# Optimization experiments

Measured on AMD Instinct MI355X. Metric: run time of the kernel, lower is better.

## Reference

```python
import jax, jax.numpy as jnp
import numpy as np
from jax import lax


def setup_inputs() -> dict:
    key = jax.random.key(0)
    k1, k2, k3, k4, k5 = jax.random.split(key, 5)
    B, T, D, N = 64, 1024, 512, 24
    return {
        "x": jax.random.normal(k1, (B, T, D), dtype=jnp.float32),
        "W": jax.random.normal(k2, (D, N), dtype=jnp.float32) * 0.05,
        "b": jnp.zeros((N,), dtype=jnp.float32),
        "trans": jax.random.normal(k3, (N, N), dtype=jnp.float32) * 0.1,
        "left_boundary": jax.random.normal(k4, (N,), dtype=jnp.float32) * 0.1,
        "right_boundary": jax.random.normal(k5, (N,), dtype=jnp.float32) * 0.1,
    }


def reference(x, W, b, trans, left_boundary, right_boundary):
    # Dense projection to tag potentials: [B, T, N]
    pot = jnp.einsum("btd,dn->btn", x, W) + b
    B, T, N = pot.shape
    # mask=None -> lengths are all T; boundaries added at t=0 and t=T-1
    lens = jnp.full((B,), T, dtype=jnp.int32)
    pot = pot.at[:, 0, :].add(left_boundary).at[:, T - 1, :].add(right_boundary)

    # Viterbi forward: alpha[b, j] = best score of any path ending in tag j
    def fwd_step(alpha, pot_t):
        scores = alpha[:, :, None] + trans[None, :, :]  # [B, prev, cur]
        bp = jnp.argmax(scores, axis=1)                 # [B, N] best prev tag
        alpha_new = jnp.max(scores, axis=1) + pot_t
        return alpha_new, bp

    alpha0 = pot[:, 0, :]
    pot_rest = jnp.swapaxes(pot[:, 1:, :], 0, 1)  # [T-1, B, N]
    alpha_T, bps = lax.scan(fwd_step, alpha0, pot_rest)
    last_tag = jnp.argmax(alpha_T, axis=-1)  # [B]

    # Backtrack through backpointers (reverse scan over time)
    def back_step(tag, bp_t):
        prev = jnp.take_along_axis(bp_t, tag[:, None], axis=1)[:, 0]
        return prev, prev

    _, tags_head = lax.scan(back_step, last_tag, bps, reverse=True)  # [T-1, B]
    decoded = jnp.concatenate(
        [jnp.swapaxes(tags_head, 0, 1), last_tag[:, None]], axis=1
    ).astype(jnp.int32)  # [B, T]
    return decoded, pot, lens, trans
```

## Files before the change

### kernel.cpp

```cpp
#include <hip/hip_runtime.h>
#include <hip/hip_bf16.h>

#define BB 64
#define TT 1024
#define DD 512
#define NS 24

#define POT_OFF   65536
#define LENS_OFF  1638400
#define TRANS_OFF 1638464

__global__ __launch_bounds__(256, 4) void gemm_pot(
    const float* __restrict__ x, const float* __restrict__ W,
    const float* __restrict__ bias, const float* __restrict__ trans,
    const float* __restrict__ lb, const float* __restrict__ rb,
    float* __restrict__ out)
{
  __shared__ float red[3][64][25];
  const int tid = threadIdx.x;
  const int l   = tid & 63;
  const int q   = __builtin_amdgcn_readfirstlane(tid >> 6);
  const int row = blockIdx.x * 64 + l;

  const float4* xp = (const float4*)(x + (size_t)row * DD + q * 128);

  float acc[NS];
#pragma unroll
  for (int nn = 0; nn < NS; ++nn) acc[nn] = 0.f;

  float4 buf[16];
#pragma unroll
  for (int i = 0; i < 16; ++i) buf[i] = xp[i];

#pragma unroll
  for (int c = 0; c < 8; ++c) {
#pragma unroll
    for (int i = 0; i < 4; ++i) {
      const int f = c * 4 + i;
      const int s = f & 15;
      float4 v = buf[s];
      if (f + 16 < 32) buf[s] = xp[f + 16];
      const float* Wr = W + (size_t)(q * 128 + f * 4) * NS;
      const float x0 = v.x, x1 = v.y, x2 = v.z, x3 = v.w;
#pragma unroll
      for (int nn = 0; nn < NS; ++nn) acc[nn] = fmaf(x0, Wr[nn],          acc[nn]);
#pragma unroll
      for (int nn = 0; nn < NS; ++nn) acc[nn] = fmaf(x1, Wr[NS + nn],     acc[nn]);
#pragma unroll
      for (int nn = 0; nn < NS; ++nn) acc[nn] = fmaf(x2, Wr[2 * NS + nn], acc[nn]);
#pragma unroll
      for (int nn = 0; nn < NS; ++nn) acc[nn] = fmaf(x3, Wr[3 * NS + nn], acc[nn]);
    }
  }

  if (q != 0) {
#pragma unroll
    for (int nn = 0; nn < NS; ++nn) red[q - 1][l][nn] = acc[nn];
  }
  __syncthreads();
  if (q == 0) {
    const int t = row & (TT - 1);
#pragma unroll
    for (int nn = 0; nn < NS; ++nn)
      acc[nn] += red[0][l][nn] + red[1][l][nn] + red[2][l][nn] + bias[nn];
    if (t == 0) {
#pragma unroll
      for (int nn = 0; nn < NS; ++nn) acc[nn] += lb[nn];
    }
    if (t == TT - 1) {
#pragma unroll
      for (int nn = 0; nn < NS; ++nn) acc[nn] += rb[nn];
    }
    float* po = out + POT_OFF + (size_t)row * NS;
#pragma unroll
    for (int i = 0; i < 6; ++i)
      *(float4*)(po + i * 4) = make_float4(acc[4*i], acc[4*i+1], acc[4*i+2], acc[4*i+3]);
  }

  if (blockIdx.x == 0 && tid < BB) out[LENS_OFF + tid] = (float)TT;
  if (blockIdx.x == 1) {
    for (int i = tid; i < NS * NS; i += 256) out[TRANS_OFF + i] = trans[i];
  }
}

__global__ __launch_bounds__(1024) void viterbi_fused(
    const float* __restrict__ pot, const float* __restrict__ trans,
    float* __restrict__ out_dec)
{
  __shared__ float ps[(TT + 8) * NS];
  __shared__ unsigned char bl[TT * NS];
  __shared__ float tl[NS * NS];
  __shared__ int H[32][NS];
  __shared__ int e[32];

  const int b = blockIdx.x, tid = threadIdx.x;

  {
    const float4* src = (const float4*)(pot + (size_t)b * TT * NS);
    float4* dst = (float4*)ps;
#pragma unroll
    for (int i = 0; i < 6; ++i) dst[tid + i * 1024] = src[tid + i * 1024];
    if (tid < NS * NS) tl[tid] = trans[tid];
  }
  __syncthreads();

  if (tid < 24) {
    const int n = tid;
    float tc[NS];
#pragma unroll
    for (int m = 0; m < NS; ++m) tc[m] = tl[m * NS + n];

    float as_[NS];
    {
      const float4* ar = (const float4*)ps;
#pragma unroll
      for (int i = 0; i < 6; ++i) {
        float4 v = ar[i];
        as_[4*i] = v.x; as_[4*i+1] = v.y; as_[4*i+2] = v.z; as_[4*i+3] = v.w;
      }
    }

    float pv[8];
#pragma unroll
    for (int u = 0; u < 8; ++u) pv[u] = ps[(1 + u) * NS + n];

    auto step = [&](int tt, float potv) {
      float sc[NS];
#pragma unroll
      for (int m = 0; m < NS; ++m) sc[m] = as_[m] + tc[m];
      float r0 = fmaxf(fmaxf(sc[0],  sc[1]),  sc[2]);
      float r1 = fmaxf(fmaxf(sc[3],  sc[4]),  sc[5]);
      float r2 = fmaxf(fmaxf(sc[6],  sc[7]),  sc[8]);
      float r3 = fmaxf(fmaxf(sc[9],  sc[10]), sc[11]);
      float r4 = fmaxf(fmaxf(sc[12], sc[13]), sc[14]);
      float r5 = fmaxf(fmaxf(sc[15], sc[16]), sc[17]);
      float r6 = fmaxf(fmaxf(sc[18], sc[19]), sc[20]);
      float r7 = fmaxf(fmaxf(sc[21], sc[22]), sc[23]);
      float q0 = fmaxf(fmaxf(r0, r1), r2);
      float q1 = fmaxf(fmaxf(r3, r4), r5);
      float q2 = fmaxf(r6, r7);
      float best = fmaxf(fmaxf(q0, q1), q2);
      float anew = best + potv;
      ps[tt * NS + n] = anew;
      const float4* ar = (const float4*)(ps + tt * NS);
#pragma unroll
      for (int i = 0; i < 6; ++i) {
        float4 v = ar[i];
        as_[4*i] = v.x; as_[4*i+1] = v.y; as_[4*i+2] = v.z; as_[4*i+3] = v.w;
      }
    };

    for (int t = 1; t + 7 <= TT - 1; t += 8) {
#pragma unroll
      for (int u = 0; u < 8; ++u) {
        const int tt = t + u;
        const float potv = pv[u];
        pv[u] = ps[(tt + 8) * NS + n];
        step(tt, potv);
      }
    }
#pragma unroll
    for (int u = 0; u < 7; ++u) step(1017 + u, pv[u]);
  }
  __syncthreads();

  for (int idx = tid; idx < (TT - 1) * NS; idx += 1024) {
    const int n = idx % NS;
    const int t = idx / NS + 1;
    const float* ar = &ps[(t - 1) * NS];
    float best = ar[0] + tl[n];
    int bi = 0;
#pragma unroll
    for (int m = 1; m < NS; ++m) {
      float s = ar[m] + tl[m * NS + n];
      bool g = s > best;
      bi = g ? m : bi;
      best = g ? s : best;
    }
    bl[t * NS + n] = (unsigned char)bi;
  }
  __syncthreads();

  if (tid < 32 * NS) {
    const int c = tid / NS, s = tid % NS;
    int a = s;
    int tlo = c * 32; if (tlo < 1) tlo = 1;
    for (int t = c * 32 + 31; t >= tlo; --t) a = bl[t * NS + a];
    H[c][s] = a;
  }
  __syncthreads();

  if (tid == 0) {
    const float* ar = &ps[(TT - 1) * NS];
    float best = ar[0]; int bi = 0;
#pragma unroll
    for (int nn = 1; nn < NS; ++nn) {
      float v = ar[nn];
      if (v > best) { best = v; bi = nn; }
    }
    int tag = bi;
    e[31] = tag;
    for (int c = 31; c >= 1; --c) { tag = H[c][tag]; e[c - 1] = tag; }
  }
  __syncthreads();

  if (tid < 32) {
    const int c = tid;
    int tag = e[c];
    float* od = out_dec + (size_t)b * TT;
    od[c * 32 + 31] = (float)tag;
    for (int t = c * 32 + 30; t >= c * 32; --t) {
      tag = bl[(t + 1) * NS + tag];
      od[t] = (float)tag;
    }
  }
}

extern "C" void kernel_launch(void* const* d_in, const int* in_sizes, int n_in,
                              void* d_out, int out_size, void* d_ws, size_t ws_size,
                              hipStream_t stream)
{
  const float* x     = (const float*)d_in[0];
  const float* W     = (const float*)d_in[1];
  const float* bias  = (const float*)d_in[2];
  const float* trans = (const float*)d_in[3];
  const float* lb    = (const float*)d_in[4];
  const float* rb    = (const float*)d_in[5];
  float* out = (float*)d_out;

  gemm_pot<<<1024, 256, 0, stream>>>(x, W, bias, trans, lb, rb, out);
  viterbi_fused<<<BB, 1024, 0, stream>>>(out + POT_OFF, trans, out);
}
```

Measured before the change: 382.6 us.

## Stage W in LDS for GEMM and split Viterbi max across two half-waves

The projection kernel now copies the whole 512x24 weight matrix into shared memory once per block and reads it as float4 rows, instead of reading W from global memory for every FMA group. The x prefetch buffer shrinks to 8 entries, and the shared buffer is reused for the cross-wave reduction. The Viterbi forward recursion now uses 64 lanes: each half-wave computes the max over 12 predecessor tags and combines with its partner through ds_bpermute, shortening the serial per-step dependency chain. Costs are 48KB of LDS per GEMM block, which limits occupancy, and an extra permute on each serial step.

Result: faster. 330.5 us (-13.6%).

```diff
diff --git a/kernel.cpp b/kernel.cpp
--- a/kernel.cpp
+++ b/kernel.cpp
@@ -10,59 +10,67 @@
 #define LENS_OFF  1638400
 #define TRANS_OFF 1638464
 
-__global__ __launch_bounds__(256, 4) void gemm_pot(
+__global__ __launch_bounds__(256) void gemm_pot(
     const float* __restrict__ x, const float* __restrict__ W,
     const float* __restrict__ bias, const float* __restrict__ trans,
     const float* __restrict__ lb, const float* __restrict__ rb,
     float* __restrict__ out)
 {
-  __shared__ float red[3][64][25];
+  __shared__ float wl[DD * NS];
   const int tid = threadIdx.x;
   const int l   = tid & 63;
-  const int q   = __builtin_amdgcn_readfirstlane(tid >> 6);
+  const int q   = tid >> 6;
   const int row = blockIdx.x * 64 + l;
 
+  {
+    const float4* Ws = (const float4*)W;
+    float4* Wd = (float4*)wl;
+#pragma unroll
+    for (int i = 0; i < 12; ++i) Wd[tid + i * 256] = Ws[tid + i * 256];
+  }
+  __syncthreads();
+
   const float4* xp = (const float4*)(x + (size_t)row * DD + q * 128);
 
   float acc[NS];
 #pragma unroll
   for (int nn = 0; nn < NS; ++nn) acc[nn] = 0.f;
 
-  float4 buf[16];
-#pragma unroll
-  for (int i = 0; i < 16; ++i) buf[i] = xp[i];
-
-#pragma unroll
-  for (int c = 0; c < 8; ++c) {
-#pragma unroll
-    for (int i = 0; i < 4; ++i) {
-      const int f = c * 4 + i;
-      const int s = f & 15;
-      float4 v = buf[s];
-      if (f + 16 < 32) buf[s] = xp[f + 16];
-      const float* Wr = W + (size_t)(q * 128 + f * 4) * NS;
-      const float x0 = v.x, x1 = v.y, x2 = v.z, x3 = v.w;
-#pragma unroll
-      for (int nn = 0; nn < NS; ++nn) acc[nn] = fmaf(x0, Wr[nn],          acc[nn]);
-#pragma unroll
-      for (int nn = 0; nn < NS; ++nn) acc[nn] = fmaf(x1, Wr[NS + nn],     acc[nn]);
-#pragma unroll
-      for (int nn = 0; nn < NS; ++nn) acc[nn] = fmaf(x2, Wr[2 * NS + nn], acc[nn]);
-#pragma unroll
-      for (int nn = 0; nn < NS; ++nn) acc[nn] = fmaf(x3, Wr[3 * NS + nn], acc[nn]);
-    }
-  }
-
+  float4 buf[8];
+#pragma unroll
+  for (int i = 0; i < 8; ++i) buf[i] = xp[i];
+
+#pragma unroll
+  for (int f = 0; f < 32; ++f) {
+    float4 v = buf[f & 7];
+    if (f + 8 < 32) buf[f & 7] = xp[f + 8];
+    const float xj[4] = {v.x, v.y, v.z, v.w};
+#pragma unroll
+    for (int j = 0; j < 4; ++j) {
+      const int k = q * 128 + f * 4 + j;
+      const float4* wr = (const float4*)&wl[k * NS];
+      float4 w0 = wr[0], w1 = wr[1], w2 = wr[2], w3 = wr[3], w4 = wr[4], w5 = wr[5];
+      const float wv[NS] = {w0.x,w0.y,w0.z,w0.w, w1.x,w1.y,w1.z,w1.w,
+                            w2.x,w2.y,w2.z,w2.w, w3.x,w3.y,w3.z,w3.w,
+                            w4.x,w4.y,w4.z,w4.w, w5.x,w5.y,w5.z,w5.w};
+      const float xv = xj[j];
+#pragma unroll
+      for (int nn = 0; nn < NS; ++nn) acc[nn] = fmaf(xv, wv[nn], acc[nn]);
+    }
+  }
+
+  __syncthreads();
   if (q != 0) {
 #pragma unroll
-    for (int nn = 0; nn < NS; ++nn) red[q - 1][l][nn] = acc[nn];
+    for (int nn = 0; nn < NS; ++nn) wl[((q - 1) * 64 + l) * 25 + nn] = acc[nn];
   }
   __syncthreads();
   if (q == 0) {
     const int t = row & (TT - 1);
 #pragma unroll
     for (int nn = 0; nn < NS; ++nn)
-      acc[nn] += red[0][l][nn] + red[1][l][nn] + red[2][l][nn] + bias[nn];
+      acc[nn] += wl[(0 * 64 + l) * 25 + nn] + wl[(1 * 64 + l) * 25 + nn]
+               + wl[(2 * 64 + l) * 25 + nn] + bias[nn];
     if (t == 0) {
 #pragma unroll
       for (int nn = 0; nn < NS; ++nn) acc[nn] += lb[nn];
@@ -104,19 +112,22 @@
   }
   __syncthreads();
 
-  if (tid < 24) {
-    const int n = tid;
-    float tc[NS];
-#pragma unroll
-    for (int m = 0; m < NS; ++m) tc[m] = tl[m * NS + n];
-
-    float as_[NS];
+  if (tid < 64) {
+    const int g  = tid >> 5;
+    const int n0 = tid & 31;
+    const int n  = (n0 < 24) ? n0 : 23;
+
+    float tc[12];
+#pragma unroll
+    for (int j = 0; j < 12; ++j) tc[j] = tl[(12 * g + j) * NS + n];
+
+    float as12[12];
     {
-      const float4* ar = (const float4*)ps;
-#pragma unroll
-      for (int i = 0; i < 6; ++i) {
-        float4 v = ar[i];
-        as_[4*i] = v.x; as_[4*i+1] = v.y; as_[4*i+2] = v.z; as_[4*i+3] = v.w;
+      const float4* rr = (const float4*)&ps[12 * g];
+#pragma unroll
+      for (int i = 0; i < 3; ++i) {
+        float4 v = rr[i];
+        as12[4*i] = v.x; as12[4*i+1] = v.y; as12[4*i+2] = v.z; as12[4*i+3] = v.w;
       }
     }
 
@@ -124,29 +135,26 @@
 #pragma unroll
     for (int u = 0; u < 8; ++u) pv[u] = ps[(1 + u) * NS + n];
 
+    const int partner = (tid ^ 32) * 4;
+
     auto step = [&](int tt, float potv) {
-      float sc[NS];
-#pragma unroll
-      for (int m = 0; m < NS; ++m) sc[m] = as_[m] + tc[m];
-      float r0 = fmaxf(fmaxf(sc[0],  sc[1]),  sc[2]);
-      float r1 = fmaxf(fmaxf(sc[3],  sc[4]),  sc[5]);
-      float r2 = fmaxf(fmaxf(sc[6],  sc[7]),  sc[8]);
-      float r3 = fmaxf(fmaxf(sc[9],  sc[10]), sc[11]);
-      float r4 = fmaxf(fmaxf(sc[12], sc[13]), sc[14]);
-      float r5 = fmaxf(fmaxf(sc[15], sc[16]), sc[17]);
-      float r6 = fmaxf(fmaxf(sc[18], sc[19]), sc[20]);
-      float r7 = fmaxf(fmaxf(sc[21], sc[22]), sc[23]);
-      float q0 = fmaxf(fmaxf(r0, r1), r2);
-      float q1 = fmaxf(fmaxf(r3, r4), r5);
-      float q2 = fmaxf(r6, r7);
-      float best = fmaxf(fmaxf(q0, q1), q2);
-      float anew = best + potv;
+      float sc[12];
+#pragma unroll
+      for (int j = 0; j < 12; ++j) sc[j] = as12[j] + tc[j];
+      float p0 = fmaxf(fmaxf(sc[0], sc[1]),  sc[2]);
+      float p1 = fmaxf(fmaxf(sc[3], sc[4]),  sc[5]);
+      float p2 = fmaxf(fmaxf(sc[6], sc[7]),  sc[8]);
+      float p3 = fmaxf(fmaxf(sc[9], sc[10]), sc[11]);
+      float pm = fmaxf(fmaxf(p0, p1), fmaxf(p2, p3));
+      float ot = __int_as_float(
+          __builtin_amdgcn_ds_bpermute(partner, __float_as_int(pm)));
+      float anew = fmaxf(pm, ot) + potv;
       ps[tt * NS + n] = anew;
-      const float4* ar = (const float4*)(ps + tt * NS);
-#pragma unroll
-      for (int i = 0; i < 6; ++i) {
-        float4 v = ar[i];
-        as_[4*i] = v.x; as_[4*i+1] = v.y; as_[4*i+2] = v.z; as_[4*i+3] = v.w;
+      const float4* rr = (const float4*)&ps[tt * NS + 12 * g];
+#pragma unroll
+      for (int i = 0; i < 3; ++i) {
+        float4 v = rr[i];
+        as12[4*i] = v.x; as12[4*i+1] = v.y; as12[4*i+2] = v.z; as12[4*i+3] = v.w;
       }
     };
 
```
